# Kernel optimization log

Hardware: AMD Instinct MI355X
Metric: run time of the kernel (lower is better)

The kernel has to match this reference:

```python
import jax, jax.numpy as jnp
import numpy as np

N_NODES = 100000
N_EDGES = 4000000
IN_DIM = 3
HID = 8
EPS = 1e-5


def _layer_norm(h, g, b):
    m = jnp.mean(h, axis=-1, keepdims=True)
    v = jnp.mean(jnp.square(h - m), axis=-1, keepdims=True)
    return (h - m) * jax.lax.rsqrt(v + EPS) * g + b


def setup_inputs() -> dict:
    key = jax.random.key(0)
    ks = jax.random.split(key, 10)
    x = jax.random.normal(ks[0], (N_NODES, IN_DIM), dtype=jnp.float32)
    edge_index = jax.random.randint(ks[1], (2, N_EDGES), 0, N_NODES, dtype=jnp.int64)

    def lin(k, fan_in, fan_out):
        bound = 1.0 / np.sqrt(fan_in)
        kw, kb = jax.random.split(k)
        W = jax.random.uniform(kw, (fan_in, fan_out), jnp.float32, -bound, bound)
        b = jax.random.uniform(kb, (fan_out,), jnp.float32, -bound, bound)
        return W, b

    W0, b0 = lin(ks[2], 2 * IN_DIM, HID)
    W1, b1 = lin(ks[3], HID, HID)
    W2, b2 = lin(ks[4], HID, HID)
    W3, b3 = lin(ks[5], HID, 1)
    g0 = jnp.ones((HID,), jnp.float32); be0 = jnp.zeros((HID,), jnp.float32)
    g1 = jnp.ones((HID,), jnp.float32); be1 = jnp.zeros((HID,), jnp.float32)
    g2 = jnp.ones((HID,), jnp.float32); be2 = jnp.zeros((HID,), jnp.float32)
    return {"x": x, "edge_index": edge_index,
            "W0": W0, "b0": b0, "g0": g0, "be0": be0,
            "W1": W1, "b1": b1, "g1": g1, "be1": be1,
            "W2": W2, "b2": b2, "g2": g2, "be2": be2,
            "W3": W3, "b3": b3}


def reference(x, edge_index, W0, b0, g0, be0, W1, b1, g1, be1, W2, b2, g2, be2, W3, b3):
    start, end = edge_index[0], edge_index[1]
    # [E, 2*IN_DIM] gathered edge inputs
    e = jnp.concatenate([x[start], x[end]], axis=1)
    h = jnp.tanh(_layer_norm(e @ W0 + b0, g0, be0))
    h = jnp.tanh(_layer_norm(h @ W1 + b1, g1, be1))
    h = jnp.tanh(_layer_norm(h @ W2 + b2, g2, be2))
    out = (h @ W3 + b3).squeeze(-1)  # [E]
    return out
```

## Files before the change

kernel.cpp:

```cpp
#include <hip/hip_runtime.h>

typedef _Float16 h2 __attribute__((ext_vector_type(2)));
typedef float f4v __attribute__((ext_vector_type(4)));
typedef f4v f4u __attribute__((aligned(4)));

#define N_EDGES 4000000
#define HID 8
#define TWO_LOG2E 2.8853900817779268f
#define LN_EPS 1e-5f

#define O_GC0 0
#define O_BC0 8
#define O_GC1 16
#define O_BC1 24
#define O_GC2 32
#define O_BC2 40
#define O_B1  48
#define O_B2  56
#define O_B3  64
#define O_W1P 72
#define O_W2P 104
#define O_W3P 136
#define O_W0P 144
#define O_B0C 176

#if __has_builtin(__builtin_amdgcn_fdot2)
#define FDOT2(a, b, c) __builtin_amdgcn_fdot2((a), (b), (c), false)
#else
#define FDOT2(a, b, c) ((float)(a)[0] * (float)(b)[0] + ((float)(a)[1] * (float)(b)[1] + (c)))
#endif

__device__ void prep_hidden_layer(const float* __restrict__ W,
                                  const float* __restrict__ b,
                                  float* __restrict__ ws, uint* __restrict__ wsu,
                                  int wofs, int bofs) {
    float Wc[64];
    for (int k = 0; k < 8; ++k) {
        float rm = 0.f;
        for (int j = 0; j < 8; ++j) rm += W[k * 8 + j];
        rm *= 0.125f;
        for (int j = 0; j < 8; ++j) Wc[k * 8 + j] = -2.f * (W[k * 8 + j] - rm);
    }
    for (int k = 0; k < 8; ++k) {
        float m = 0.f;
        for (int j = 0; j < 8; ++j) m += (float)(_Float16)Wc[k * 8 + j];
        m *= 0.125f;
        for (int j = 0; j < 8; ++j) Wc[k * 8 + j] -= m;
    }
    for (int j = 0; j < 8; ++j)
        for (int q = 0; q < 4; ++q) {
            h2 v;
            v[0] = (_Float16)Wc[(2 * q) * 8 + j];
            v[1] = (_Float16)Wc[(2 * q + 1) * 8 + j];
            wsu[wofs + j * 4 + q] = __builtin_bit_cast(uint, v);
        }
    float mb = 0.f, tot = 0.f;
    for (int j = 0; j < 8; ++j) mb += b[j];
    for (int i = 0; i < 64; ++i) tot += W[i];
    for (int j = 0; j < 8; ++j) {
        float cs = 0.f;
        for (int k = 0; k < 8; ++k) cs += W[k * 8 + j];
        ws[bofs + j] = b[j] + cs - mb * 0.125f - tot * 0.125f;
    }
}

__global__ void prep_kernel(
    const float* __restrict__ W0, const float* __restrict__ b0,
    const float* __restrict__ g0, const float* __restrict__ be0,
    const float* __restrict__ W1, const float* __restrict__ b1,
    const float* __restrict__ g1, const float* __restrict__ be1,
    const float* __restrict__ W2, const float* __restrict__ b2,
    const float* __restrict__ g2, const float* __restrict__ be2,
    const float* __restrict__ W3, const float* __restrict__ b3,
    float* __restrict__ ws)
{
    const int t = threadIdx.x;
    uint* wsu = reinterpret_cast<uint*>(ws);

    if (t == 0) {
        for (int j = 0; j < 8; ++j) {
            ws[O_GC0 + j] = g0[j] * TWO_LOG2E;  ws[O_BC0 + j] = be0[j] * TWO_LOG2E;
            ws[O_GC1 + j] = g1[j] * TWO_LOG2E;  ws[O_BC1 + j] = be1[j] * TWO_LOG2E;
            ws[O_GC2 + j] = g2[j] * TWO_LOG2E;  ws[O_BC2 + j] = be2[j] * TWO_LOG2E;
        }
    } else if (t == 1) {
        float Wc[48];
        for (int k = 0; k < 6; ++k) {
            float rm = 0.f;
            for (int j = 0; j < 8; ++j) rm += W0[k * 8 + j];
            rm *= 0.125f;
            for (int j = 0; j < 8; ++j) Wc[k * 8 + j] = W0[k * 8 + j] - rm;
        }
        for (int k = 0; k < 6; ++k) {
            float m = 0.f;
            for (int j = 0; j < 8; ++j) m += (float)(_Float16)Wc[k * 8 + j];
            m *= 0.125f;
            for (int j = 0; j < 8; ++j) Wc[k * 8 + j] -= m;
        }
        for (int j = 0; j < 8; ++j) {
            h2 v;
            v[0] = (_Float16)Wc[0 * 8 + j]; v[1] = (_Float16)Wc[1 * 8 + j];
            wsu[O_W0P + j * 4 + 0] = __builtin_bit_cast(uint, v);
            v[0] = (_Float16)Wc[2 * 8 + j]; v[1] = (_Float16)0.f;
            wsu[O_W0P + j * 4 + 1] = __builtin_bit_cast(uint, v);
            v[0] = (_Float16)Wc[3 * 8 + j]; v[1] = (_Float16)Wc[4 * 8 + j];
            wsu[O_W0P + j * 4 + 2] = __builtin_bit_cast(uint, v);
            v[0] = (_Float16)Wc[5 * 8 + j]; v[1] = (_Float16)0.f;
            wsu[O_W0P + j * 4 + 3] = __builtin_bit_cast(uint, v);
        }
        float bm = 0.f;
        for (int j = 0; j < 8; ++j) bm += b0[j];
        bm *= 0.125f;
        for (int j = 0; j < 8; ++j) ws[O_B0C + j] = b0[j] - bm;
    } else if (t == 2) {
        prep_hidden_layer(W1, b1, ws, wsu, O_W1P, O_B1);
    } else if (t == 3) {
        prep_hidden_layer(W2, b2, ws, wsu, O_W2P, O_B2);
    } else if (t == 4) {
        float s = 0.f;
        for (int k = 0; k < 8; ++k) s += W3[k];
        ws[O_B3] = b3[0] + s;
        for (int q = 0; q < 4; ++q) {
            h2 v;
            v[0] = (_Float16)(-2.f * W3[2 * q]);
            v[1] = (_Float16)(-2.f * W3[2 * q + 1]);
            wsu[O_W3P + q] = __builtin_bit_cast(uint, v);
        }
    }
}

__global__ __launch_bounds__(256, 8) void edge_mlp_kernel(
    const float* __restrict__ x,
    const int*   __restrict__ ei,
    const float* __restrict__ ws,
    float* __restrict__ out)
{
    const uint t = blockIdx.x * 256u + threadIdx.x;
    if (t >= N_EDGES) return;

    const uint* wsu = reinterpret_cast<const uint*>(ws);
    const uint s = (uint)ei[t];
    const uint d = (uint)ei[N_EDGES + t];

    const f4u vsrc = *reinterpret_cast<const f4u*>(x + s * 3u);
    const f4u vdst = *reinterpret_cast<const f4u*>(x + d * 3u);

    const h2 s01 = __builtin_bit_cast(h2, __builtin_amdgcn_cvt_pkrtz(vsrc[0], vsrc[1]));
    const h2 s2z = __builtin_bit_cast(h2, __builtin_amdgcn_cvt_pkrtz(vsrc[2], 0.f));
    const h2 d01 = __builtin_bit_cast(h2, __builtin_amdgcn_cvt_pkrtz(vdst[0], vdst[1]));
    const h2 d2z = __builtin_bit_cast(h2, __builtin_amdgcn_cvt_pkrtz(vdst[2], 0.f));

    float z[HID];
#pragma unroll
    for (int j = 0; j < HID; ++j) {
        const h2 wj0 = __builtin_bit_cast(h2, wsu[O_W0P + j * 4 + 0]);
        const h2 wj1 = __builtin_bit_cast(h2, wsu[O_W0P + j * 4 + 1]);
        const h2 wj2 = __builtin_bit_cast(h2, wsu[O_W0P + j * 4 + 2]);
        const h2 wj3 = __builtin_bit_cast(h2, wsu[O_W0P + j * 4 + 3]);
        float a = FDOT2(s01, wj0, ws[O_B0C + j]);
        a = FDOT2(s2z, wj1, a);
        a = FDOT2(d01, wj2, a);
        z[j] = FDOT2(d2z, wj3, a);
    }

    h2 p[4];
    const int gco[3] = {O_GC0, O_GC1, O_GC2};
    const int bco[3] = {O_BC0, O_BC1, O_BC2};
    const int wpo[2] = {O_W1P, O_W2P};
    const int bpo[2] = {O_B1, O_B2};

#pragma unroll
    for (int L = 0; L < 3; ++L) {
        float va = 0.f;
#pragma unroll
        for (int j = 0; j < HID; ++j) va = __builtin_fmaf(z[j], z[j], va);
        const float r = __builtin_amdgcn_rsqf(__builtin_fmaf(va, 0.125f, LN_EPS));
        const float* gc = ws + gco[L];
        const float* bc = ws + bco[L];
        float e1[HID];
#pragma unroll
        for (int j = 0; j < HID; ++j) {
            const float y = __builtin_fmaf(z[j], r * gc[j], bc[j]);
            e1[j] = __builtin_amdgcn_exp2f(y) + 1.0f;
        }
#pragma unroll
        for (int q = 0; q < 4; ++q) {
            const float a = e1[2 * q], b = e1[2 * q + 1];
            const float pr = __builtin_amdgcn_rcpf(a * b);
            p[q] = __builtin_bit_cast(h2,
                __builtin_amdgcn_cvt_pkrtz(b * pr, a * pr));
        }
        if (L < 2) {
            const uint* wp = wsu + wpo[L];
            const float* bb = ws + bpo[L];
#pragma unroll
            for (int j = 0; j < HID; ++j) {
                float acc = FDOT2(p[0], __builtin_bit_cast(h2, wp[j * 4 + 0]), bb[j]);
                acc = FDOT2(p[1], __builtin_bit_cast(h2, wp[j * 4 + 1]), acc);
                acc = FDOT2(p[2], __builtin_bit_cast(h2, wp[j * 4 + 2]), acc);
                z[j] = FDOT2(p[3], __builtin_bit_cast(h2, wp[j * 4 + 3]), acc);
            }
        }
    }

    float acc = FDOT2(p[0], __builtin_bit_cast(h2, wsu[O_W3P + 0]), ws[O_B3]);
    acc = FDOT2(p[1], __builtin_bit_cast(h2, wsu[O_W3P + 1]), acc);
    acc = FDOT2(p[2], __builtin_bit_cast(h2, wsu[O_W3P + 2]), acc);
    out[t] = FDOT2(p[3], __builtin_bit_cast(h2, wsu[O_W3P + 3]), acc);
}

extern "C" void kernel_launch(void* const* d_in, const int* in_sizes, int n_in,
                              void* d_out, int out_size, void* d_ws, size_t ws_size,
                              hipStream_t stream) {
    const float* x   = (const float*)d_in[0];
    const int*   ei  = (const int*)d_in[1];
    const float* W0  = (const float*)d_in[2];
    const float* b0  = (const float*)d_in[3];
    const float* g0  = (const float*)d_in[4];
    const float* be0 = (const float*)d_in[5];
    const float* W1  = (const float*)d_in[6];
    const float* b1  = (const float*)d_in[7];
    const float* g1  = (const float*)d_in[8];
    const float* be1 = (const float*)d_in[9];
    const float* W2  = (const float*)d_in[10];
    const float* b2  = (const float*)d_in[11];
    const float* g2  = (const float*)d_in[12];
    const float* be2 = (const float*)d_in[13];
    const float* W3  = (const float*)d_in[14];
    const float* b3  = (const float*)d_in[15];
    float* out = (float*)d_out;
    float* ws  = (float*)d_ws;

    prep_kernel<<<1, 64, 0, stream>>>(W0, b0, g0, be0, W1, b1, g1, be1,
                                      W2, b2, g2, be2, W3, b3, ws);

    const int blocks = (N_EDGES + 255) / 256;
    edge_mlp_kernel<<<blocks, 256, 0, stream>>>(x, ei, ws, out);
}
```

Before: 54.94 us.

## Process two edges per thread and stage weights in shared memory

Each thread now handles two edges, using vectorized int2 index loads and a float2 store, and reuses each loaded weight for both edges. The packed weights are copied into LDS once per block and read from there instead of through scalar global loads. This cuts per-edge weight-load and index-load overhead and exposes more independent ALU work per thread. In exchange it adds a block barrier, halves the thread count, and raises register pressure, which may lower occupancy.

```diff
diff --git a/kernel.cpp b/kernel.cpp
--- a/kernel.cpp
+++ b/kernel.cpp
@@ -6,6 +6,7 @@
 
 #define N_EDGES 4000000
 #define HID 8
+#define NPT 2
 #define TWO_LOG2E 2.8853900817779268f
 #define LN_EPS 1e-5f
 
@@ -23,6 +24,7 @@
 #define O_W3P 136
 #define O_W0P 144
 #define O_B0C 176
+#define NW    192
 
 #if __has_builtin(__builtin_amdgcn_fdot2)
 #define FDOT2(a, b, c) __builtin_amdgcn_fdot2((a), (b), (c), false)
@@ -135,35 +137,51 @@
     const float* __restrict__ ws,
     float* __restrict__ out)
 {
+    __shared__ float lw[NW];
+    if (threadIdx.x < NW) lw[threadIdx.x] = ws[threadIdx.x];
+    __syncthreads();
+    const uint* lwu = reinterpret_cast<const uint*>(lw);
+
     const uint t = blockIdx.x * 256u + threadIdx.x;
-    if (t >= N_EDGES) return;
-
-    const uint* wsu = reinterpret_cast<const uint*>(ws);
-    const uint s = (uint)ei[t];
-    const uint d = (uint)ei[N_EDGES + t];
-
-    const f4u vsrc = *reinterpret_cast<const f4u*>(x + s * 3u);
-    const f4u vdst = *reinterpret_cast<const f4u*>(x + d * 3u);
-
-    const h2 s01 = __builtin_bit_cast(h2, __builtin_amdgcn_cvt_pkrtz(vsrc[0], vsrc[1]));
-    const h2 s2z = __builtin_bit_cast(h2, __builtin_amdgcn_cvt_pkrtz(vsrc[2], 0.f));
-    const h2 d01 = __builtin_bit_cast(h2, __builtin_amdgcn_cvt_pkrtz(vdst[0], vdst[1]));
-    const h2 d2z = __builtin_bit_cast(h2, __builtin_amdgcn_cvt_pkrtz(vdst[2], 0.f));
-
-    float z[HID];
+    const uint base = t * NPT;
+    if (base >= N_EDGES) return;
+
+    const int2 sv = *reinterpret_cast<const int2*>(ei + base);
+    const int2 dv = *reinterpret_cast<const int2*>(ei + N_EDGES + base);
+
+    const f4u vs0 = *reinterpret_cast<const f4u*>(x + (uint)sv.x * 3u);
+    const f4u vs1 = *reinterpret_cast<const f4u*>(x + (uint)sv.y * 3u);
+    const f4u vd0 = *reinterpret_cast<const f4u*>(x + (uint)dv.x * 3u);
+    const f4u vd1 = *reinterpret_cast<const f4u*>(x + (uint)dv.y * 3u);
+
+    h2 s01[NPT], s2z[NPT], d01[NPT], d2z[NPT];
+    s01[0] = __builtin_bit_cast(h2, __builtin_amdgcn_cvt_pkrtz(vs0[0], vs0[1]));
+    s2z[0] = __builtin_bit_cast(h2, __builtin_amdgcn_cvt_pkrtz(vs0[2], 0.f));
+    d01[0] = __builtin_bit_cast(h2, __builtin_amdgcn_cvt_pkrtz(vd0[0], vd0[1]));
+    d2z[0] = __builtin_bit_cast(h2, __builtin_amdgcn_cvt_pkrtz(vd0[2], 0.f));
+    s01[1] = __builtin_bit_cast(h2, __builtin_amdgcn_cvt_pkrtz(vs1[0], vs1[1]));
+    s2z[1] = __builtin_bit_cast(h2, __builtin_amdgcn_cvt_pkrtz(vs1[2], 0.f));
+    d01[1] = __builtin_bit_cast(h2, __builtin_amdgcn_cvt_pkrtz(vd1[0], vd1[1]));
+    d2z[1] = __builtin_bit_cast(h2, __builtin_amdgcn_cvt_pkrtz(vd1[2], 0.f));
+
+    float z[NPT][HID];
 #pragma unroll
     for (int j = 0; j < HID; ++j) {
-        const h2 wj0 = __builtin_bit_cast(h2, wsu[O_W0P + j * 4 + 0]);
-        const h2 wj1 = __builtin_bit_cast(h2, wsu[O_W0P + j * 4 + 1]);
-        const h2 wj2 = __builtin_bit_cast(h2, wsu[O_W0P + j * 4 + 2]);
-        const h2 wj3 = __builtin_bit_cast(h2, wsu[O_W0P + j * 4 + 3]);
-        float a = FDOT2(s01, wj0, ws[O_B0C + j]);
-        a = FDOT2(s2z, wj1, a);
-        a = FDOT2(d01, wj2, a);
-        z[j] = FDOT2(d2z, wj3, a);
-    }
-
-    h2 p[4];
+        const h2 wj0 = __builtin_bit_cast(h2, lwu[O_W0P + j * 4 + 0]);
+        const h2 wj1 = __builtin_bit_cast(h2, lwu[O_W0P + j * 4 + 1]);
+        const h2 wj2 = __builtin_bit_cast(h2, lwu[O_W0P + j * 4 + 2]);
+        const h2 wj3 = __builtin_bit_cast(h2, lwu[O_W0P + j * 4 + 3]);
+        const float bb = lw[O_B0C + j];
+#pragma unroll
+        for (int e = 0; e < NPT; ++e) {
+            float a = FDOT2(s01[e], wj0, bb);
+            a = FDOT2(s2z[e], wj1, a);
+            a = FDOT2(d01[e], wj2, a);
+            z[e][j] = FDOT2(d2z[e], wj3, a);
+        }
+    }
+
+    h2 p[NPT][4];
     const int gco[3] = {O_GC0, O_GC1, O_GC2};
     const int bco[3] = {O_BC0, O_BC1, O_BC2};
     const int wpo[2] = {O_W1P, O_W2P};
@@ -171,42 +189,71 @@
 
 #pragma unroll
     for (int L = 0; L < 3; ++L) {
-        float va = 0.f;
-#pragma unroll
-        for (int j = 0; j < HID; ++j) va = __builtin_fmaf(z[j], z[j], va);
-        const float r = __builtin_amdgcn_rsqf(__builtin_fmaf(va, 0.125f, LN_EPS));
-        const float* gc = ws + gco[L];
-        const float* bc = ws + bco[L];
-        float e1[HID];
+        float r[NPT];
+#pragma unroll
+        for (int e = 0; e < NPT; ++e) {
+            float va = 0.f;
+#pragma unroll
+            for (int j = 0; j < HID; ++j) va = __builtin_fmaf(z[e][j], z[e][j], va);
+            r[e] = __builtin_amdgcn_rsqf(__builtin_fmaf(va, 0.125f, LN_EPS));
+        }
+        const float* gc = lw + gco[L];
+        const float* bc = lw + bco[L];
+        float e1[NPT][HID];
 #pragma unroll
         for (int j = 0; j < HID; ++j) {
-            const float y = __builtin_fmaf(z[j], r * gc[j], bc[j]);
-            e1[j] = __builtin_amdgcn_exp2f(y) + 1.0f;
-        }
-#pragma unroll
-        for (int q = 0; q < 4; ++q) {
-            const float a = e1[2 * q], b = e1[2 * q + 1];
-            const float pr = __builtin_amdgcn_rcpf(a * b);
-            p[q] = __builtin_bit_cast(h2,
-                __builtin_amdgcn_cvt_pkrtz(b * pr, a * pr));
-        }
+            const float gcj = gc[j], bcj = bc[j];
+#pragma unroll
+            for (int e = 0; e < NPT; ++e) {
+                const float y = __builtin_fmaf(z[e][j], r[e] * gcj, bcj);
+                e1[e][j] = __builtin_amdgcn_exp2f(y) + 1.0f;
+            }
+        }
+#pragma unroll
+        for (int q = 0; q < 4; ++q)
+#pragma unroll
+            for (int e = 0; e < NPT; ++e) {
+                const float a = e1[e][2 * q], b = e1[e][2 * q + 1];
+                const float pr = __builtin_amdgcn_rcpf(a * b);
+                p[e][q] = __builtin_bit_cast(h2,
+                    __builtin_amdgcn_cvt_pkrtz(b * pr, a * pr));
+            }
         if (L < 2) {
-            const uint* wp = wsu + wpo[L];
-            const float* bb = ws + bpo[L];
+            const uint* wp = lwu + wpo[L];
+            const float* bb = lw + bpo[L];
 #pragma unroll
             for (int j = 0; j < HID; ++j) {
-                float acc = FDOT2(p[0], __builtin_bit_cast(h2, wp[j * 4 + 0]), bb[j]);
-                acc = FDOT2(p[1], __builtin_bit_cast(h2, wp[j * 4 + 1]), acc);
-                acc = FDOT2(p[2], __builtin_bit_cast(h2, wp[j * 4 + 2]), acc);
-                z[j] = FDOT2(p[3], __builtin_bit_cast(h2, wp[j * 4 + 3]), acc);
+                const h2 w0 = __builtin_bit_cast(h2, wp[j * 4 + 0]);
+                const h2 w1 = __builtin_bit_cast(h2, wp[j * 4 + 1]);
+                const h2 w2 = __builtin_bit_cast(h2, wp[j * 4 + 2]);
+                const h2 w3 = __builtin_bit_cast(h2, wp[j * 4 + 3]);
+                const float bj = bb[j];
+#pragma unroll
+                for (int e = 0; e < NPT; ++e) {
+                    float acc = FDOT2(p[e][0], w0, bj);
+                    acc = FDOT2(p[e][1], w1, acc);
+                    acc = FDOT2(p[e][2], w2, acc);
+                    z[e][j] = FDOT2(p[e][3], w3, acc);
+                }
             }
         }
     }
 
-    float acc = FDOT2(p[0], __builtin_bit_cast(h2, wsu[O_W3P + 0]), ws[O_B3]);
-    acc = FDOT2(p[1], __builtin_bit_cast(h2, wsu[O_W3P + 1]), acc);
-    acc = FDOT2(p[2], __builtin_bit_cast(h2, wsu[O_W3P + 2]), acc);
-    out[t] = FDOT2(p[3], __builtin_bit_cast(h2, wsu[O_W3P + 3]), acc);
+    const h2 w30 = __builtin_bit_cast(h2, lwu[O_W3P + 0]);
+    const h2 w31 = __builtin_bit_cast(h2, lwu[O_W3P + 1]);
+    const h2 w32 = __builtin_bit_cast(h2, lwu[O_W3P + 2]);
+    const h2 w33 = __builtin_bit_cast(h2, lwu[O_W3P + 3]);
+    const float bb3 = lw[O_B3];
+    float o[NPT];
+#pragma unroll
+    for (int e = 0; e < NPT; ++e) {
+        float acc = FDOT2(p[e][0], w30, bb3);
+        acc = FDOT2(p[e][1], w31, acc);
+        acc = FDOT2(p[e][2], w32, acc);
+        o[e] = FDOT2(p[e][3], w33, acc);
+    }
+
+    *reinterpret_cast<float2*>(out + base) = make_float2(o[0], o[1]);
 }
 
 extern "C" void kernel_launch(void* const* d_in, const int* in_sizes, int n_in,
@@ -234,6 +281,7 @@
     prep_kernel<<<1, 64, 0, stream>>>(W0, b0, g0, be0, W1, b1, g1, be1,
                                       W2, b2, g2, be2, W3, b3, ws);
 
-    const int blocks = (N_EDGES + 255) / 256;
+    const int nthreads = N_EDGES / NPT;
+    const int blocks = (nthreads + 255) / 256;
     edge_mlp_kernel<<<blocks, 256, 0, stream>>>(x, ei, ws, out);
 }
```

Result: slower. 87.75 us (+59.7%).
